# Kernel tuning notes

Measured on AMD Instinct MI355X. Metric: run time of the kernel, lower is better.

The kernel has to match this reference:

```python
import jax, jax.numpy as jnp
import numpy as np

B, T, D, V = 32, 2048, 256, 2048  # batch, time, embed_dim, num_codebooks


def setup_inputs() -> dict:
    key = jax.random.key(0)
    k1, k2 = jax.random.split(key)
    z = jax.random.normal(k1, (B, T, D), dtype=jnp.float32)
    codebook_weight = jax.random.normal(k2, (V, D), dtype=jnp.float32)
    return {"z": z, "codebook_weight": codebook_weight}


def reference(z, codebook_weight):
    # e = codebook.embedding.weight.clone().detach()
    e = jax.lax.stop_gradient(codebook_weight)            # (V, D)
    zf = z.reshape(-1, e.shape[1])                        # (N, D), N = B*T
    # squared euclidean distances via GEMM expansion
    d = (jnp.sum(zf * zf, axis=1, keepdims=True)
         + jnp.sum(e * e, axis=1)
         - 2.0 * zf @ e.T)                                # (N, V)
    idx = jnp.argmin(d, axis=1)                           # (N,)
    # one-hot matmul with e is mathematically a row gather of e
    z_q = jnp.take(e, idx, axis=0).reshape(z.shape)       # (B, T, D)
    commitment_loss = jnp.mean((z - jax.lax.stop_gradient(z_q)) ** 2)
    z_q_st = z + jax.lax.stop_gradient(z_q - z)           # straight-through
    encoding_indices = idx.reshape(z.shape[0], z.shape[1])  # (B, T)
    hist = jnp.bincount(idx, length=V).astype(jnp.float32)
    codebook_prob = hist / (hist.sum() + 1e-8)
    return commitment_loss, z_q_st, encoding_indices, codebook_prob
```

## Files before the change

### kernel.cpp

```cpp
#include <hip/hip_runtime.h>

#define NROWS 65536
#define DIM   256
#define VCB   2048
#define DELTA 0.25f

typedef _Float16 f16;
typedef _Float16 f16x8 __attribute__((ext_vector_type(8)));
typedef float    f32x4 __attribute__((ext_vector_type(4)));


__device__ __forceinline__ void async16(void* lds, const void* g) {
  __builtin_amdgcn_global_load_lds(
      (const __attribute__((address_space(1))) void*)g,
      (__attribute__((address_space(3))) void*)lds, 16, 0, 0);
}

__global__ __launch_bounds__(256) void convert_kernel(
    const float4* __restrict__ src, short4* __restrict__ dhi,
    short4* __restrict__ dlo, int n4) {
  int stride = gridDim.x * 256;
  for (int i = blockIdx.x * 256 + threadIdx.x; i < n4; i += stride) {
    float4 v = src[i];
    union { f16 h[4]; short4 s; } H, L;
    H.h[0] = (f16)v.x; H.h[1] = (f16)v.y; H.h[2] = (f16)v.z; H.h[3] = (f16)v.w;
    L.h[0] = (f16)(v.x - (float)H.h[0]);
    L.h[1] = (f16)(v.y - (float)H.h[1]);
    L.h[2] = (f16)(v.z - (float)H.h[2]);
    L.h[3] = (f16)(v.w - (float)H.h[3]);
    dhi[i] = H.s; dlo[i] = L.s;
  }
}

__global__ __launch_bounds__(256) void prep_kernel(
    const float* __restrict__ e, float* __restrict__ enorm,
    unsigned int* __restrict__ hist, double* __restrict__ loss_part,
    int* __restrict__ flag_cnt) {
  int tid = threadIdx.x;
  int gt = blockIdx.x * 256 + tid;
  if (gt == 0) flag_cnt[0] = 0;
  if (gt < VCB) hist[gt] = 0u;
  if (gt < 256) loss_part[gt] = 0.0;
  int wid  = gt >> 6;
  int lane = tid & 63;
  if (wid < VCB) {
    const float4* row = (const float4*)(e + (size_t)wid * DIM);
    float4 v = row[lane];
    float s = v.x*v.x + v.y*v.y + v.z*v.z + v.w*v.w;
    #pragma unroll
    for (int off = 32; off; off >>= 1) s += __shfl_xor(s, off);
    if (lane == 0) enorm[wid] = s;
  }
}

__global__ __launch_bounds__(512) void pass1_kernel(
    const float* __restrict__ z, const f16* __restrict__ eh,
    const float* __restrict__ enorm,
    int* __restrict__ idx_out, unsigned int* __restrict__ hist,
    double* __restrict__ loss_part,
    int* __restrict__ flag_cnt, int* __restrict__ flag_list) {
  __shared__ f16 ldsA[8][4096];
  __shared__ f16 ldsB[2][16384];
  __shared__ float sx1[3][2][64];
  __shared__ float sx2[3][2][64];
  __shared__ int   sxi[3][2][64];

  const int tid  = threadIdx.x;
  const int wid  = tid >> 6;
  const int lane = tid & 63;
  const int wr   = wid >> 2;
  const int wc   = wid & 3;
  const int lrow = lane & 15;
  const int lq   = lane >> 4;
  const int rbase = blockIdx.x * 128;

  const int srow = tid >> 2;
  const int scol = tid & 3;
  const int skoff = ((scol ^ ((srow >> 1) & 3)) << 3);

  auto stageB = [&](int b, int ss, int kh) {
    #pragma unroll
    for (int s = 0; s < 4; ++s) {
      size_t goff = (size_t)(ss * 128 + srow) * DIM + kh * 128 + s * 32 + skoff;
      async16(&ldsB[b][s * 4096] + tid * 8, eh + goff);
    }
  };

  {
    const int row = tid >> 2;
    const int q   = tid & 3;
    const float* zrow = z + (size_t)(rbase + row) * DIM + q * 64;
    const int sw = (row >> 1) & 3;
    float zs = 0.f;
    #pragma unroll
    for (int f = 0; f < 16; ++f) {
      float4 v = *(const float4*)(zrow + f * 4);
      int col4   = q * 64 + f * 4;
      int kt     = col4 >> 5;
      int ko     = col4 & 31;
      int chunk  = ko >> 3;
      int within = (ko & 7) * 2;
      int addr = kt * 8192 + row * 64 + ((chunk ^ sw) << 4) + within;
      union { f16 h[4]; short4 s4; } H;
      H.h[0] = (f16)v.x; H.h[1] = (f16)v.y; H.h[2] = (f16)v.z; H.h[3] = (f16)v.w;
      *(short4*)((char*)ldsA + addr) = H.s4;
      zs += v.x*v.x + v.y*v.y + v.z*v.z + v.w*v.w;
    }
    #pragma unroll
    for (int off = 32; off; off >>= 1) zs += __shfl_xor(zs, off);
    if (lane == 0) atomicAdd(&loss_part[blockIdx.x & 255], (double)zs);
  }
  stageB(0, 0, 0);
  asm volatile("s_waitcnt vmcnt(0)" ::: "memory");
  __syncthreads();

  float m1[4][4], m2v[4][4];
  int   i1[4][4];
  #pragma unroll
  for (int m = 0; m < 4; ++m)
    #pragma unroll
    for (int r = 0; r < 4; ++r) { m1[m][r] = 3.4e38f; m2v[m][r] = 3.4e38f; i1[m][r] = 0; }

  const int cchunk = lq ^ ((lrow >> 1) & 3);

  int pb = 0;
  for (int ss = 0; ss < 16; ++ss) {
    f32x4 acc[4][2];
    #pragma unroll
    for (int m = 0; m < 4; ++m)
      #pragma unroll
      for (int n = 0; n < 2; ++n) {
        f32x4 zz = {0.f, 0.f, 0.f, 0.f};
        acc[m][n] = zz;
      }

    for (int kh = 0; kh < 2; ++kh) {
      bool last = (ss == 15) && (kh == 1);
      if (!last) {
        int nkh = kh + 1, nss = ss;
        if (nkh == 2) { nkh = 0; ++nss; }
        stageB(pb ^ 1, nss, nkh);
        asm volatile("s_waitcnt vmcnt(4)" ::: "memory");
      } else {
        asm volatile("s_waitcnt vmcnt(0)" ::: "memory");
      }
      asm volatile("s_barrier" ::: "memory");
      __builtin_amdgcn_sched_barrier(0);

      #pragma unroll
      for (int kp = 0; kp < 4; ++kp) {
        const char* abase = (const char*)&ldsA[kh * 4 + kp][0];
        f16x8 ah[4];
        #pragma unroll
        for (int m = 0; m < 4; ++m) {
          int row = wr * 64 + m * 16 + lrow;
          ah[m] = *(const f16x8*)(abase + row * 64 + cchunk * 16);
        }
        const char* bbase = (const char*)&ldsB[pb][kp * 4096];
        #pragma unroll
        for (int n = 0; n < 2; ++n) {
          int col = wc * 32 + n * 16 + lrow;
          f16x8 bh = *(const f16x8*)(bbase + col * 64 + cchunk * 16);
          #pragma unroll
          for (int m = 0; m < 4; ++m)
            acc[m][n] = __builtin_amdgcn_mfma_f32_16x16x32_f16(ah[m], bh, acc[m][n], 0, 0, 0);
        }
      }
      __builtin_amdgcn_sched_barrier(0);
      asm volatile("s_barrier" ::: "memory");
      pb ^= 1;
    }

    #pragma unroll
    for (int n = 0; n < 2; ++n) {
      int j = ss * 128 + wc * 32 + n * 16 + lrow;
      float en = enorm[j];
      #pragma unroll
      for (int m = 0; m < 4; ++m)
        #pragma unroll
        for (int r = 0; r < 4; ++r) {
          float s = fmaf(-2.f, acc[m][n][r], en);
          if (s < m1[m][r]) { m2v[m][r] = m1[m][r]; m1[m][r] = s; i1[m][r] = j; }
          else if (s < m2v[m][r]) m2v[m][r] = s;
        }
    }
  }

  #pragma unroll
  for (int off = 1; off < 16; off <<= 1) {
    #pragma unroll
    for (int m = 0; m < 4; ++m)
      #pragma unroll
      for (int r = 0; r < 4; ++r) {
        float o1 = __shfl_xor(m1[m][r], off);
        int   oi = __shfl_xor(i1[m][r], off);
        float o2 = __shfl_xor(m2v[m][r], off);
        float nm2 = fminf(fminf(m2v[m][r], o2), fmaxf(m1[m][r], o1));
        if (o1 < m1[m][r] || (o1 == m1[m][r] && oi < i1[m][r])) {
          m1[m][r] = o1; i1[m][r] = oi;
        }
        m2v[m][r] = nm2;
      }
  }

  if (wc != 0 && lrow == 0) {
    #pragma unroll
    for (int m = 0; m < 4; ++m)
      #pragma unroll
      for (int r = 0; r < 4; ++r) {
        int li = m * 16 + lq * 4 + r;
        sx1[wc - 1][wr][li] = m1[m][r];
        sx2[wc - 1][wr][li] = m2v[m][r];
        sxi[wc - 1][wr][li] = i1[m][r];
      }
  }
  __syncthreads();
  if (wc == 0 && lrow == 0) {
    float lsum = 0.f;
    #pragma unroll
    for (int m = 0; m < 4; ++m)
      #pragma unroll
      for (int r = 0; r < 4; ++r) {
        int li = m * 16 + lq * 4 + r;
        float v  = m1[m][r];
        int   bi = i1[m][r];
        float v2 = m2v[m][r];
        #pragma unroll
        for (int g = 0; g < 3; ++g) {
          float ov = sx1[g][wr][li];
          float o2 = sx2[g][wr][li];
          int   oi = sxi[g][wr][li];
          float nm2 = fminf(fminf(v2, o2), fmaxf(v, ov));
          if (ov < v || (ov == v && oi < bi)) { v = ov; bi = oi; }
          v2 = nm2;
        }
        int row = rbase + wr * 64 + li;
        if (v2 - v <= DELTA) {
          int p = atomicAdd(flag_cnt, 1);
          flag_list[p] = row;
        } else {
          idx_out[row] = bi;
          atomicAdd(&hist[bi], 1u);
          lsum += v;
        }
      }
    lsum += __shfl_xor(lsum, 16);
    lsum += __shfl_xor(lsum, 32);
    if (lane == 0) atomicAdd(&loss_part[blockIdx.x & 255], (double)lsum);
  }
}

__global__ __launch_bounds__(512) void pass2_kernel(
    const float* __restrict__ z,
    const f16* __restrict__ eh, const f16* __restrict__ el,
    const float* __restrict__ enorm,
    const int* __restrict__ flag_cnt, const int* __restrict__ flag_list,
    float* __restrict__ pval, int* __restrict__ pidx) {
  __shared__ f16 ldsA[8][8192];
  __shared__ f16 ldsB[2][8192];

  const int tid  = threadIdx.x;
  const int wid  = tid >> 6;
  const int lane = tid & 63;
  const int wr   = wid >> 2;
  const int wc   = wid & 3;
  const int lrow = lane & 15;
  const int lq   = lane >> 4;
  const int srow = tid >> 2;
  const int scol = tid & 3;
  const int skoff = ((scol ^ ((srow >> 1) & 3)) << 3);
  const int cchunk = lq ^ ((lrow >> 1) & 3);
  const int cnt = *flag_cnt;

  auto stageB = [&](int b, int vcol, int kt) {
    size_t off = (size_t)(vcol + srow) * DIM + (kt << 5) + skoff;
    async16(&ldsB[b][0]    + tid * 8, eh + off);
    async16(&ldsB[b][4096] + tid * 8, el + off);
  };

  for (int job = blockIdx.x; ; job += gridDim.x) {
    int chunk = job >> 4, cb = job & 15;
    int base = chunk * 128;
    if (base >= cnt) break;
    int nrows = cnt - base; if (nrows > 128) nrows = 128;

    __syncthreads();

    {
      const int row = tid >> 2;
      const int q   = tid & 3;
      int grow = flag_list[base + (row < nrows ? row : 0)];
      const float* zrow = z + (size_t)grow * DIM + q * 64;
      const int sw = (row >> 1) & 3;
      #pragma unroll
      for (int f = 0; f < 16; ++f) {
        float4 v = *(const float4*)(zrow + f * 4);
        int col4   = q * 64 + f * 4;
        int kt     = col4 >> 5;
        int ko     = col4 & 31;
        int chunk2 = ko >> 3;
        int within = (ko & 7) * 2;
        int addr = kt * 16384 + row * 64 + ((chunk2 ^ sw) << 4) + within;
        union { f16 h[4]; short4 s4; } H, L;
        H.h[0] = (f16)v.x; H.h[1] = (f16)v.y; H.h[2] = (f16)v.z; H.h[3] = (f16)v.w;
        L.h[0] = (f16)(v.x - (float)H.h[0]);
        L.h[1] = (f16)(v.y - (float)H.h[1]);
        L.h[2] = (f16)(v.z - (float)H.h[2]);
        L.h[3] = (f16)(v.w - (float)H.h[3]);
        *(short4*)((char*)ldsA + addr)        = H.s4;
        *(short4*)((char*)ldsA + addr + 8192) = L.s4;
      }
    }
    int pb = 0;
    stageB(0, cb * 128, 0);
    asm volatile("s_waitcnt vmcnt(0)" ::: "memory");
    __syncthreads();

    float minv[4][4];
    int   mini[4][4];
    #pragma unroll
    for (int m = 0; m < 4; ++m)
      #pragma unroll
      for (int r = 0; r < 4; ++r) { minv[m][r] = 3.4e38f; mini[m][r] = 0; }

    f32x4 acc[4][2];
    #pragma unroll
    for (int m = 0; m < 4; ++m)
      #pragma unroll
      for (int n = 0; n < 2; ++n) {
        f32x4 zz = {0.f, 0.f, 0.f, 0.f};
        acc[m][n] = zz;
      }

    for (int kt = 0; kt < 8; ++kt) {
      if (kt < 7) {
        stageB(pb ^ 1, cb * 128, kt + 1);
        asm volatile("s_waitcnt vmcnt(2)" ::: "memory");
      } else {
        asm volatile("s_waitcnt vmcnt(0)" ::: "memory");
      }
      asm volatile("s_barrier" ::: "memory");
      __builtin_amdgcn_sched_barrier(0);

      const char* abase = (const char*)&ldsA[kt][0];
      f16x8 ah[4], al[4];
      #pragma unroll
      for (int m = 0; m < 4; ++m) {
        int row = wr * 64 + m * 16 + lrow;
        int off = row * 64 + cchunk * 16;
        ah[m] = *(const f16x8*)(abase + off);
        al[m] = *(const f16x8*)(abase + 8192 + off);
      }
      const char* bbase = (const char*)&ldsB[pb][0];
      #pragma unroll
      for (int n = 0; n < 2; ++n) {
        int col = wc * 32 + n * 16 + lrow;
        int off = col * 64 + cchunk * 16;
        f16x8 bh = *(const f16x8*)(bbase + off);
        f16x8 bl = *(const f16x8*)(bbase + 8192 + off);
        #pragma unroll
        for (int m = 0; m < 4; ++m) {
          acc[m][n] = __builtin_amdgcn_mfma_f32_16x16x32_f16(ah[m], bh, acc[m][n], 0, 0, 0);
          acc[m][n] = __builtin_amdgcn_mfma_f32_16x16x32_f16(ah[m], bl, acc[m][n], 0, 0, 0);
          acc[m][n] = __builtin_amdgcn_mfma_f32_16x16x32_f16(al[m], bh, acc[m][n], 0, 0, 0);
        }
      }
      __builtin_amdgcn_sched_barrier(0);
      asm volatile("s_barrier" ::: "memory");
      pb ^= 1;
    }

    #pragma unroll
    for (int n = 0; n < 2; ++n) {
      int j = cb * 128 + wc * 32 + n * 16 + lrow;
      float en = enorm[j];
      #pragma unroll
      for (int m = 0; m < 4; ++m)
        #pragma unroll
        for (int r = 0; r < 4; ++r) {
          float s = fmaf(-2.f, acc[m][n][r], en);
          if (s < minv[m][r]) { minv[m][r] = s; mini[m][r] = j; }
        }
    }

    #pragma unroll
    for (int off = 1; off < 16; off <<= 1) {
      #pragma unroll
      for (int m = 0; m < 4; ++m)
        #pragma unroll
        for (int r = 0; r < 4; ++r) {
          float ov = __shfl_xor(minv[m][r], off);
          int   oi = __shfl_xor(mini[m][r], off);
          if (ov < minv[m][r] || (ov == minv[m][r] && oi < mini[m][r])) {
            minv[m][r] = ov; mini[m][r] = oi;
          }
        }
    }

    __syncthreads();
    float* sxv = (float*)&ldsB[0][0];
    int*   sxi2 = (int*)(sxv + 3 * 2 * 64);
    if (wc != 0 && lrow == 0) {
      #pragma unroll
      for (int m = 0; m < 4; ++m)
        #pragma unroll
        for (int r = 0; r < 4; ++r) {
          int li = m * 16 + lq * 4 + r;
          int ix = ((wc - 1) * 2 + wr) * 64 + li;
          sxv[ix] = minv[m][r];
          sxi2[ix] = mini[m][r];
        }
    }
    __syncthreads();
    if (wc == 0 && lrow == 0) {
      #pragma unroll
      for (int m = 0; m < 4; ++m)
        #pragma unroll
        for (int r = 0; r < 4; ++r) {
          int li = m * 16 + lq * 4 + r;
          float v  = minv[m][r];
          int   bi = mini[m][r];
          #pragma unroll
          for (int g = 0; g < 3; ++g) {
            int ix = (g * 2 + wr) * 64 + li;
            float ov = sxv[ix];
            int   oi = sxi2[ix];
            if (ov < v || (ov == v && oi < bi)) { v = ov; bi = oi; }
          }
          int i = wr * 64 + li;
          if (i < nrows) {
            int fi = base + i;
            pval[fi * 16 + cb] = v;
            pidx[fi * 16 + cb] = bi;
          }
        }
    }
  }
}

__global__ __launch_bounds__(256) void pass2m_kernel(
    const int* __restrict__ flag_cnt, const int* __restrict__ flag_list,
    const float* __restrict__ pval, const int* __restrict__ pidx,
    int* __restrict__ idx_out, unsigned int* __restrict__ hist,
    double* __restrict__ loss_part) {
  int cnt = *flag_cnt;
  int t = blockIdx.x * 256 + threadIdx.x;
  int stride = gridDim.x * 256;
  for (int fi = t; fi < cnt; fi += stride) {
    float m = 3.4e38f; int bi = 0;
    #pragma unroll
    for (int cb = 0; cb < 16; ++cb) {
      float v = pval[fi * 16 + cb];
      int  ix = pidx[fi * 16 + cb];
      if (v < m || (v == m && ix < bi)) { m = v; bi = ix; }
    }
    int row = flag_list[fi];
    idx_out[row] = bi;
    atomicAdd(&hist[bi], 1u);
    atomicAdd(&loss_part[fi & 255], (double)m);
  }
}

__global__ __launch_bounds__(256) void gather_kernel(
    const float* __restrict__ e, const int* __restrict__ idx,
    float* __restrict__ zq_out, float* __restrict__ idxf_out) {
  int tid  = threadIdx.x;
  int w    = tid >> 6;
  int lane = tid & 63;
  int n    = blockIdx.x * 4 + w;

  int ci = idx[n];
  const float4* er = (const float4*)(e + (size_t)ci * DIM);
  ((float4*)(zq_out + (size_t)n * DIM))[lane] = er[lane];
  if (lane == 0) idxf_out[n] = (float)ci;
}

__global__ __launch_bounds__(256) void finalize_kernel(
    const unsigned int* __restrict__ hist, const double* __restrict__ loss_part,
    float* __restrict__ out) {
  __shared__ double lsh[4];
  __shared__ float  hsh[4];
  __shared__ float  denom_sh;
  int tid = threadIdx.x, lane = tid & 63, w = tid >> 6;

  float hs = 0.f;
  for (int j = tid; j < VCB; j += 256) hs += (float)hist[j];
  double ls = loss_part[tid];
  #pragma unroll
  for (int off = 32; off; off >>= 1) {
    hs += __shfl_xor(hs, off);
    ls += __shfl_xor(ls, off);
  }
  if (lane == 0) { lsh[w] = ls; hsh[w] = hs; }
  __syncthreads();
  if (tid == 0) {
    double lt = lsh[0] + lsh[1] + lsh[2] + lsh[3];
    float  ht = hsh[0] + hsh[1] + hsh[2] + hsh[3];
    out[0] = (float)(lt / (double)((size_t)NROWS * DIM));
    denom_sh = ht + 1e-8f;
  }
  __syncthreads();
  float denom = denom_sh;
  float* prob = out + 1 + (size_t)NROWS * DIM + NROWS;
  for (int j = tid; j < VCB; j += 256) prob[j] = (float)hist[j] / denom;
}

extern "C" void kernel_launch(void* const* d_in, const int* in_sizes, int n_in,
                              void* d_out, int out_size, void* d_ws, size_t ws_size,
                              hipStream_t stream) {
  (void)in_sizes; (void)n_in; (void)out_size; (void)ws_size;
  const float* z = (const float*)d_in[0];
  const float* e = (const float*)d_in[1];
  float* out = (float*)d_out;
  char*  ws  = (char*)d_ws;

  int*          idx       = (int*)ws;
  unsigned int* hist      = (unsigned int*)(ws + 262144);
  double*       loss_part = (double*)(ws + 270336);
  float*        enorm     = (float*)(ws + 272384);
  int*          flag_cnt  = (int*)(ws + 280576);
  f16*          e_hi      = (f16*)(ws + 524288);
  f16*          e_lo      = (f16*)(ws + 1572864);

  float* pval      = out + 32;
  int*   pidx      = (int*)(out + 32 + 1048576);
  int*   flag_list = (int*)(out + 32 + 2097152);

  float* out_zq  = out + 1;
  float* out_idx = out + 1 + (size_t)NROWS * DIM;

  convert_kernel<<<128, 256, 0, stream>>>(
      (const float4*)e, (short4*)e_hi, (short4*)e_lo, VCB * DIM / 4);
  prep_kernel<<<512, 256, 0, stream>>>(e, enorm, hist, loss_part, flag_cnt);
  pass1_kernel<<<NROWS / 128, 512, 0, stream>>>(
      z, e_hi, enorm, idx, hist, loss_part, flag_cnt, flag_list);
  pass2_kernel<<<512, 512, 0, stream>>>(
      z, e_hi, e_lo, enorm, flag_cnt, flag_list, pval, pidx);
  pass2m_kernel<<<64, 256, 0, stream>>>(
      flag_cnt, flag_list, pval, pidx, idx, hist, loss_part);
  gather_kernel<<<NROWS / 4, 256, 0, stream>>>(e, idx, out_zq, out_idx);
  finalize_kernel<<<1, 256, 0, stream>>>(hist, loss_part, out);
}
```

Baseline: 222.4 us.

## Use 256-wide codebook tiles with triple-buffered single-barrier B staging

```diff
diff --git a/kernel.cpp b/kernel.cpp
--- a/kernel.cpp
+++ b/kernel.cpp
@@ -60,7 +60,7 @@
     double* __restrict__ loss_part,
     int* __restrict__ flag_cnt, int* __restrict__ flag_list) {
   __shared__ f16 ldsA[8][4096];
-  __shared__ f16 ldsB[2][16384];
+  __shared__ f16 ldsB[3][8192];
   __shared__ float sx1[3][2][64];
   __shared__ float sx2[3][2][64];
   __shared__ int   sxi[3][2][64];
@@ -74,15 +74,14 @@
   const int lq   = lane >> 4;
   const int rbase = blockIdx.x * 128;
 
-  const int srow = tid >> 2;
-  const int scol = tid & 3;
-  const int skoff = ((scol ^ ((srow >> 1) & 3)) << 3);
-
-  auto stageB = [&](int b, int ss, int kh) {
-    #pragma unroll
-    for (int s = 0; s < 4; ++s) {
-      size_t goff = (size_t)(ss * 128 + srow) * DIM + kh * 128 + s * 32 + skoff;
-      async16(&ldsB[b][s * 4096] + tid * 8, eh + goff);
+  auto stageB = [&](int b, int ss, int kt) {
+    #pragma unroll
+    for (int i = 0; i < 2; ++i) {
+      int col   = wid * 32 + i * 16 + (lane >> 2);
+      int chunk = lane & 3;
+      int gk    = chunk ^ ((col >> 1) & 3);
+      size_t goff = (size_t)(ss * 256 + col) * DIM + (kt << 5) + (gk << 3);
+      async16(&ldsB[b][0] + col * 32 + chunk * 8, eh + goff);
     }
   };
 
@@ -124,56 +123,47 @@
   const int cchunk = lq ^ ((lrow >> 1) & 3);
 
   int pb = 0;
-  for (int ss = 0; ss < 16; ++ss) {
-    f32x4 acc[4][2];
+  for (int ss = 0; ss < 8; ++ss) {
+    f32x4 acc[4][4];
     #pragma unroll
     for (int m = 0; m < 4; ++m)
       #pragma unroll
-      for (int n = 0; n < 2; ++n) {
+      for (int n = 0; n < 4; ++n) {
         f32x4 zz = {0.f, 0.f, 0.f, 0.f};
         acc[m][n] = zz;
       }
 
-    for (int kh = 0; kh < 2; ++kh) {
-      bool last = (ss == 15) && (kh == 1);
-      if (!last) {
-        int nkh = kh + 1, nss = ss;
-        if (nkh == 2) { nkh = 0; ++nss; }
-        stageB(pb ^ 1, nss, nkh);
-        asm volatile("s_waitcnt vmcnt(4)" ::: "memory");
-      } else {
-        asm volatile("s_waitcnt vmcnt(0)" ::: "memory");
-      }
+    for (int kt = 0; kt < 8; ++kt) {
+      int nkt = kt + 1, nss = ss;
+      if (nkt == 8) { nkt = 0; ++nss; if (nss == 8) nss = 0; }
+      int nxt = pb + 1; if (nxt == 3) nxt = 0;
+      stageB(nxt, nss, nkt);
+      asm volatile("s_waitcnt vmcnt(2)" ::: "memory");
       asm volatile("s_barrier" ::: "memory");
       __builtin_amdgcn_sched_barrier(0);
 
-      #pragma unroll
-      for (int kp = 0; kp < 4; ++kp) {
-        const char* abase = (const char*)&ldsA[kh * 4 + kp][0];
-        f16x8 ah[4];
-        #pragma unroll
-        for (int m = 0; m < 4; ++m) {
-          int row = wr * 64 + m * 16 + lrow;
-          ah[m] = *(const f16x8*)(abase + row * 64 + cchunk * 16);
-        }
-        const char* bbase = (const char*)&ldsB[pb][kp * 4096];
-        #pragma unroll
-        for (int n = 0; n < 2; ++n) {
-          int col = wc * 32 + n * 16 + lrow;
-          f16x8 bh = *(const f16x8*)(bbase + col * 64 + cchunk * 16);
-          #pragma unroll
-          for (int m = 0; m < 4; ++m)
-            acc[m][n] = __builtin_amdgcn_mfma_f32_16x16x32_f16(ah[m], bh, acc[m][n], 0, 0, 0);
-        }
-      }
-      __builtin_amdgcn_sched_barrier(0);
-      asm volatile("s_barrier" ::: "memory");
-      pb ^= 1;
-    }
-
-    #pragma unroll
-    for (int n = 0; n < 2; ++n) {
-      int j = ss * 128 + wc * 32 + n * 16 + lrow;
+      const char* abase = (const char*)&ldsA[kt][0];
+      f16x8 ah[4];
+      #pragma unroll
+      for (int m = 0; m < 4; ++m) {
+        int row = wr * 64 + m * 16 + lrow;
+        ah[m] = *(const f16x8*)(abase + row * 64 + cchunk * 16);
+      }
+      const char* bbase = (const char*)&ldsB[pb][0];
+      #pragma unroll
+      for (int n = 0; n < 4; ++n) {
+        int col = wc * 64 + n * 16 + lrow;
+        f16x8 bh = *(const f16x8*)(bbase + col * 64 + cchunk * 16);
+        #pragma unroll
+        for (int m = 0; m < 4; ++m)
+          acc[m][n] = __builtin_amdgcn_mfma_f32_16x16x32_f16(ah[m], bh, acc[m][n], 0, 0, 0);
+      }
+      pb = nxt;
+    }
+
+    #pragma unroll
+    for (int n = 0; n < 4; ++n) {
+      int j = ss * 256 + wc * 64 + n * 16 + lrow;
       float en = enorm[j];
       #pragma unroll
       for (int m = 0; m < 4; ++m)
@@ -185,6 +175,7 @@
         }
     }
   }
+  asm volatile("s_waitcnt vmcnt(0)" ::: "memory");
 
   #pragma unroll
   for (int off = 1; off < 16; off <<= 1) {
@@ -203,6 +194,7 @@
       }
   }
 
+  __syncthreads();
   if (wc != 0 && lrow == 0) {
     #pragma unroll
     for (int m = 0; m < 4; ++m)
```

After: 212.6 us. -4.4%, faster.
